# Kernel optimization log

Hardware: AMD Instinct MI355X
Metric: run time of the kernel (lower is better)

The kernel has to match this reference:

```python
import jax, jax.numpy as jnp
import numpy as np

B, T, N = 1024, 256, 64  # batch, seq_len, n_labels


def setup_inputs() -> dict:
    key = jax.random.key(0)
    k1, k2, k3, k4, k5 = jax.random.split(key, 5)
    emit = jax.random.normal(k1, (B, T, N), dtype=jnp.float32)
    lens = jax.random.randint(k2, (B,), T // 2, T + 1)
    mask = jnp.arange(T)[None, :] < lens[:, None]  # [B, T] bool, monotone
    trans = 0.1 * jax.random.normal(k3, (N, N), dtype=jnp.float32)
    strans = 0.1 * jax.random.normal(k4, (N,), dtype=jnp.float32)
    etrans = 0.1 * jax.random.normal(k5, (N,), dtype=jnp.float32)
    return {"emit": emit, "trans": trans, "strans": strans,
            "etrans": etrans, "mask": mask}


def reference(emit, trans, strans, etrans, mask):
    """CRF partition function (Tagger.get_logZ), summed over the batch."""
    lse = jax.scipy.special.logsumexp
    # row-normalize transitions in log space (as in the torch module)
    strans_n = strans - lse(strans)
    etrans_n = etrans - lse(etrans)
    trans_n = trans - lse(trans, axis=-1, keepdims=True)  # [N, N]

    e = jnp.transpose(emit, (1, 0, 2))  # [T, B, N]
    m = mask.T                          # [T, B]

    alpha0 = strans_n + e[0]            # [B, N]

    def step(alpha, xs):
        emit_t, mask_t = xs             # [B, N], [B]
        # scores[b, k] = logsumexp_j(alpha[b, j] + trans[j, k] + emit_t[b, k])
        scores = lse(alpha[:, :, None] + trans_n[None, :, :]
                     + emit_t[:, None, :], axis=1)
        alpha = jnp.where(mask_t[:, None], scores, alpha)
        return alpha, None

    alpha, _ = jax.lax.scan(step, alpha0, (e[1:], m[1:]))
    logZ = jnp.sum(lse(alpha + etrans_n, axis=1))
    return logZ
```

## Files before the change

kernel.cpp:

```cpp
#include <hip/hip_runtime.h>


#define CRF_B 1024
#define CRF_T 256
#define CRF_N 64

typedef __bf16 bf16x2 __attribute__((ext_vector_type(2)));

__device__ __forceinline__ float rl0(float x) {
    return __int_as_float(__builtin_amdgcn_readfirstlane(__float_as_int(x)));
}
__device__ __forceinline__ float rlanef(float x, int j) {
    return __int_as_float(__builtin_amdgcn_readlane(__float_as_int(x), j));
}

__device__ __forceinline__ float wave_lse(float v) {
    float m = v;
    #pragma unroll
    for (int off = 1; off < 64; off <<= 1) m = fmaxf(m, __shfl_xor(m, off));
    float s = __expf(v - m);
    #pragma unroll
    for (int off = 1; off < 64; off <<= 1) s += __shfl_xor(s, off);
    return m + __logf(s);
}

__device__ __forceinline__ unsigned bf16_rne(float f) {
    unsigned u = __float_as_uint(f);
    return (u + 0x7FFFu + ((u >> 16) & 1u)) >> 16;
}

__device__ __forceinline__ float dot2bf(unsigned a, unsigned b, float c) {
#if __has_builtin(__builtin_amdgcn_fdot2_f32_bf16)
    return __builtin_amdgcn_fdot2_f32_bf16(__builtin_bit_cast(bf16x2, a),
                                           __builtin_bit_cast(bf16x2, b),
                                           c, false);
#else
    float d = c;
    asm("v_dot2_f32_bf16 %0, %1, %2, %0" : "+v"(d) : "v"(a), "v"(b));
    return d;
#endif
}

__launch_bounds__(64, 1)
__global__ void crf_fwd_kernel(const float* __restrict__ emit,
                               const float* __restrict__ trans,
                               const float* __restrict__ strans,
                               const float* __restrict__ etrans,
                               const unsigned char* __restrict__ mask_u8,
                               float* __restrict__ out)
{
    const int lane = threadIdx.x;
    const int b    = blockIdx.x;

    __shared__ __attribute__((aligned(16))) unsigned s_up[32];

    float rowlse_v;
    {
        const float* rowp = trans + lane * CRF_N;
        float m = -1e30f;
        #pragma unroll 8
        for (int k = 0; k < CRF_N; ++k) m = fmaxf(m, rowp[k]);
        float s = 0.f;
        #pragma unroll 8
        for (int k = 0; k < CRF_N; ++k) s += __expf(rowp[k] - m);
        rowlse_v = m + __logf(s);
    }

    float cmx = -1e30f;
    #pragma unroll
    for (int j = 0; j < CRF_N; ++j)
        cmx = fmaxf(cmx, trans[j * CRF_N + lane] - rlanef(rowlse_v, j));

    unsigned Epk[32];
    #pragma unroll
    for (int m = 0; m < 32; ++m) {
        float e0 = __expf(trans[(2 * m)     * CRF_N + lane] - rlanef(rowlse_v, 2 * m)     - cmx);
        float e1 = __expf(trans[(2 * m + 1) * CRF_N + lane] - rlanef(rowlse_v, 2 * m + 1) - cmx);
        Epk[m] = bf16_rne(e0) | (bf16_rne(e1) << 16);
    }

    const float sn = wave_lse(strans[lane]);

    int len;
    {
        int c8 = 0;
        #pragma unroll
        for (int q = 0; q < 4; ++q)
            c8 += (mask_u8[(size_t)b * CRF_T + q * 64 + lane] != 0) ? 1 : 0;
        for (int off = 1; off < 64; off <<= 1) c8 += __shfl_xor(c8, off);
        if (c8 >= 128) {
            len = c8;
        } else {
            const int* mi = (const int*)mask_u8;
            int ci = 0;
            #pragma unroll
            for (int q = 0; q < 4; ++q)
                ci += (mi[(size_t)b * CRF_T + q * 64 + lane] != 0) ? 1 : 0;
            for (int off = 1; off < 64; off <<= 1) ci += __shfl_xor(ci, off);
            len = ci;
        }
    }

    const float* eb = emit + (size_t)b * CRF_T * CRF_N;

    float alpha0 = (strans[lane] - sn) + eb[lane];
    float c0 = rl0(alpha0);
    float u  = __expf(alpha0 - c0);
    ((unsigned short*)s_up)[lane] =
        (unsigned short)((__float_as_uint(u) + 0x8000u) >> 16);
    float R  = 1.0f;
    float Pm = 1.0f;
    int   Eacc = 0;

#define CRF_STEP(EE, EE0)                                                   \
    {                                                                       \
        float ree = R * (EE);               \
        float sc0 = R * (EE0);                                              \
        float a0 = 0.f, a1 = 0.f, a2 = 0.f, a3 = 0.f;                       \
        _Pragma("unroll")                                                   \
        for (int m2 = 0; m2 < 32; m2 += 4) {                                \
            uint4 w = *(const uint4*)&s_up[m2];     \
            a0 = dot2bf(w.x, Epk[m2 + 0], a0);                              \
            a1 = dot2bf(w.y, Epk[m2 + 1], a1);                              \
            a2 = dot2bf(w.z, Epk[m2 + 2], a2);                              \
            a3 = dot2bf(w.w, Epk[m2 + 3], a3);                              \
        }                                                                   \
        float s = (a0 + a1) + (a2 + a3);                                    \
        float s0 = rl0(s);                                                  \
        u = s * ree;                                                        \
        ((unsigned short*)s_up)[lane] =                                     \
            (unsigned short)((__float_as_uint(u) + 0x8000u) >> 16);         \
        float u0 = s0 * sc0;              \
        R = __builtin_amdgcn_rcpf(u0);                                      \
        Pm *= u0;                                                           \
    }

    float eN[4], eeC[4], ee0C[4];
    #pragma unroll
    for (int d = 0; d < 4; ++d) eN[d] = eb[(size_t)(1 + d) * CRF_N + lane];
    #pragma unroll
    for (int d = 0; d < 4; ++d) eeC[d] = __expf(eN[d] + cmx);
    #pragma unroll
    for (int d = 0; d < 4; ++d) ee0C[d] = rl0(eeC[d]);

    int t0 = 1;
    while (t0 + 4 <= len) {
        #pragma unroll
        for (int d = 0; d < 4; ++d) {
            int ti = t0 + 4 + d;
            ti = (ti < len) ? ti : (len - 1);
            eN[d] = eb[(size_t)ti * CRF_N + lane];
        }
        CRF_STEP(eeC[0], ee0C[0]); CRF_STEP(eeC[1], ee0C[1]);
        CRF_STEP(eeC[2], ee0C[2]); CRF_STEP(eeC[3], ee0C[3]);
        {
            int ex;
            Pm = frexpf(Pm, &ex);
            Eacc += ex;
        }
        #pragma unroll
        for (int d = 0; d < 4; ++d) eeC[d] = __expf(eN[d] + cmx);
        #pragma unroll
        for (int d = 0; d < 4; ++d) ee0C[d] = rl0(eeC[d]);
        t0 += 4;
    }
    {
        const int nrem = len - t0;
        #pragma unroll
        for (int d = 0; d < 4; ++d) {
            if (d >= nrem) break;
            CRF_STEP(eeC[d], ee0C[d]);
        }
    }
#undef CRF_STEP

    const float en = wave_lse(etrans[lane]);
    float Lacc = c0 + 0.6931471805599453f * (float)Eacc + __logf(Pm);
    float v = Lacc + __logf(u * R) + (etrans[lane] - en);
    float m = v;
    #pragma unroll
    for (int off = 1; off < 64; off <<= 1) m = fmaxf(m, __shfl_xor(m, off));
    float sum = __expf(v - m);
    #pragma unroll
    for (int off = 1; off < 64; off <<= 1) sum += __shfl_xor(sum, off);

    if (lane == 0) {
        atomicAdd(out, m + __logf(sum));
    }
}

extern "C" void kernel_launch(void* const* d_in, const int* in_sizes, int n_in,
                              void* d_out, int out_size, void* d_ws, size_t ws_size,
                              hipStream_t stream) {
    const float* emit   = (const float*)d_in[0];
    const float* trans  = (const float*)d_in[1];
    const float* strans = (const float*)d_in[2];
    const float* etrans = (const float*)d_in[3];
    const unsigned char* mask = (const unsigned char*)d_in[4];
    float* out = (float*)d_out;

    hipMemsetAsync(out, 0, sizeof(float), stream);
    crf_fwd_kernel<<<dim3(CRF_B), dim3(64), 0, stream>>>(
        emit, trans, strans, etrans, mask, out);
}
```

Measured before the change: 144.5 us.

## Split CRF matvec between readlane broadcast and LDS, deepen emission prefetch

Each step now builds packed bf16 pairs in registers with a DPP swap and a perm. The first half of the 64-element dot product takes its operands through scalar readlane broadcasts, while the second half still reads LDS; the LDS write moves to the start of the step. This aims to hide LDS store-to-load latency on the serial recurrence, and the dot products now run over eight accumulators instead of four. Emission loads are also prefetched one group further ahead and interleaved step by step with the exp and readfirstlane work. In exchange it adds many readlane instructions per step and relies on the LDS write being visible to the wave's own later LDS reads without an explicit barrier.

```diff
diff --git a/kernel.cpp b/kernel.cpp
--- a/kernel.cpp
+++ b/kernel.cpp
@@ -27,6 +27,13 @@
 __device__ __forceinline__ unsigned bf16_rne(float f) {
     unsigned u = __float_as_uint(f);
     return (u + 0x7FFFu + ((u >> 16) & 1u)) >> 16;
+}
+
+__device__ __forceinline__ unsigned pack_pairs(float u) {
+    unsigned pa = __float_as_uint(u) + 0x8000u;
+    unsigned pb = (unsigned)__builtin_amdgcn_update_dpp(
+        0, (int)pa, 0xB1 , 0xF, 0xF, false);
+    return __builtin_amdgcn_perm(pb, pa, 0x07060302);
 }
 
 __device__ __forceinline__ float dot2bf(unsigned a, unsigned b, float c) {
@@ -116,25 +123,68 @@
     {                                                                       \
         float ree = R * (EE);               \
         float sc0 = R * (EE0);                                              \
+           \
+        ((unsigned short*)s_up)[lane] =                                     \
+            (unsigned short)((__float_as_uint(u) + 0x8000u) >> 16);         \
+        unsigned upi_ = pack_pairs(u);                                      \
+                           \
+        uint4 w4 = *(const uint4*)&s_up[16];                                \
+        uint4 w5 = *(const uint4*)&s_up[20];                                \
+        uint4 w6 = *(const uint4*)&s_up[24];                                \
+        uint4 w7 = *(const uint4*)&s_up[28];                                \
         float a0 = 0.f, a1 = 0.f, a2 = 0.f, a3 = 0.f;                       \
-        _Pragma("unroll")                                                   \
-        for (int m2 = 0; m2 < 32; m2 += 4) {                                \
-            uint4 w = *(const uint4*)&s_up[m2];     \
-            a0 = dot2bf(w.x, Epk[m2 + 0], a0);                              \
-            a1 = dot2bf(w.y, Epk[m2 + 1], a1);                              \
-            a2 = dot2bf(w.z, Epk[m2 + 2], a2);                              \
-            a3 = dot2bf(w.w, Epk[m2 + 3], a3);                              \
-        }                                                                   \
-        float s = (a0 + a1) + (a2 + a3);                                    \
+        float a4 = 0.f, a5 = 0.f, a6 = 0.f, a7 = 0.f;                       \
+                                    \
+        a0 = dot2bf((unsigned)__builtin_amdgcn_readlane((int)upi_,  0), Epk[ 0], a0); \
+        a1 = dot2bf((unsigned)__builtin_amdgcn_readlane((int)upi_,  2), Epk[ 1], a1); \
+        a2 = dot2bf((unsigned)__builtin_amdgcn_readlane((int)upi_,  4), Epk[ 2], a2); \
+        a3 = dot2bf((unsigned)__builtin_amdgcn_readlane((int)upi_,  6), Epk[ 3], a3); \
+        a4 = dot2bf((unsigned)__builtin_amdgcn_readlane((int)upi_,  8), Epk[ 4], a4); \
+        a5 = dot2bf((unsigned)__builtin_amdgcn_readlane((int)upi_, 10), Epk[ 5], a5); \
+        a6 = dot2bf((unsigned)__builtin_amdgcn_readlane((int)upi_, 12), Epk[ 6], a6); \
+        a7 = dot2bf((unsigned)__builtin_amdgcn_readlane((int)upi_, 14), Epk[ 7], a7); \
+        a0 = dot2bf((unsigned)__builtin_amdgcn_readlane((int)upi_, 16), Epk[ 8], a0); \
+        a1 = dot2bf((unsigned)__builtin_amdgcn_readlane((int)upi_, 18), Epk[ 9], a1); \
+        a2 = dot2bf((unsigned)__builtin_amdgcn_readlane((int)upi_, 20), Epk[10], a2); \
+        a3 = dot2bf((unsigned)__builtin_amdgcn_readlane((int)upi_, 22), Epk[11], a3); \
+        a4 = dot2bf((unsigned)__builtin_amdgcn_readlane((int)upi_, 24), Epk[12], a4); \
+        a5 = dot2bf((unsigned)__builtin_amdgcn_readlane((int)upi_, 26), Epk[13], a5); \
+        a6 = dot2bf((unsigned)__builtin_amdgcn_readlane((int)upi_, 28), Epk[14], a6); \
+        a7 = dot2bf((unsigned)__builtin_amdgcn_readlane((int)upi_, 30), Epk[15], a7); \
+            \
+        a0 = dot2bf(w4.x, Epk[16], a0);                                     \
+        a1 = dot2bf(w4.y, Epk[17], a1);                                     \
+        a2 = dot2bf(w4.z, Epk[18], a2);                                     \
+        a3 = dot2bf(w4.w, Epk[19], a3);                                     \
+        a4 = dot2bf(w5.x, Epk[20], a4);                                     \
+        a5 = dot2bf(w5.y, Epk[21], a5);                                     \
+        a6 = dot2bf(w5.z, Epk[22], a6);                                     \
+        a7 = dot2bf(w5.w, Epk[23], a7);                                     \
+        a0 = dot2bf(w6.x, Epk[24], a0);                                     \
+        a1 = dot2bf(w6.y, Epk[25], a1);                                     \
+        a2 = dot2bf(w6.z, Epk[26], a2);                                     \
+        a3 = dot2bf(w6.w, Epk[27], a3);                                     \
+        a4 = dot2bf(w7.x, Epk[28], a4);                                     \
+        a5 = dot2bf(w7.y, Epk[29], a5);                                     \
+        a6 = dot2bf(w7.z, Epk[30], a6);                                     \
+        a7 = dot2bf(w7.w, Epk[31], a7);                                     \
+        float s = (((a0 + a1) + (a2 + a3)) + ((a4 + a5) + (a6 + a7)));      \
         float s0 = rl0(s);                                                  \
         u = s * ree;                                                        \
-        ((unsigned short*)s_up)[lane] =                                     \
-            (unsigned short)((__float_as_uint(u) + 0x8000u) >> 16);         \
         float u0 = s0 * sc0;              \
         R = __builtin_amdgcn_rcpf(u0);                                      \
         Pm *= u0;                                                           \
     }
 
+#define CRF_ROT(D)                                                          \
+    {                                                                       \
+        eeC[D]  = __expf(eN[D] + cmx);                                      \
+        ee0C[D] = rl0(eeC[D]);                                              \
+        int ti = t0 + 8 + (D);                                              \
+        ti = (ti < len) ? ti : (len - 1);                                   \
+        eN[D] = eb[(size_t)ti * CRF_N + lane];                              \
+    }
+
     float eN[4], eeC[4], ee0C[4];
     #pragma unroll
     for (int d = 0; d < 4; ++d) eN[d] = eb[(size_t)(1 + d) * CRF_N + lane];
@@ -142,26 +192,20 @@
     for (int d = 0; d < 4; ++d) eeC[d] = __expf(eN[d] + cmx);
     #pragma unroll
     for (int d = 0; d < 4; ++d) ee0C[d] = rl0(eeC[d]);
+    #pragma unroll
+    for (int d = 0; d < 4; ++d) eN[d] = eb[(size_t)(5 + d) * CRF_N + lane];
 
     int t0 = 1;
     while (t0 + 4 <= len) {
-        #pragma unroll
-        for (int d = 0; d < 4; ++d) {
-            int ti = t0 + 4 + d;
-            ti = (ti < len) ? ti : (len - 1);
-            eN[d] = eb[(size_t)ti * CRF_N + lane];
-        }
-        CRF_STEP(eeC[0], ee0C[0]); CRF_STEP(eeC[1], ee0C[1]);
-        CRF_STEP(eeC[2], ee0C[2]); CRF_STEP(eeC[3], ee0C[3]);
+        CRF_STEP(eeC[0], ee0C[0]); CRF_ROT(0);
+        CRF_STEP(eeC[1], ee0C[1]); CRF_ROT(1);
+        CRF_STEP(eeC[2], ee0C[2]); CRF_ROT(2);
+        CRF_STEP(eeC[3], ee0C[3]); CRF_ROT(3);
         {
             int ex;
             Pm = frexpf(Pm, &ex);
             Eacc += ex;
         }
-        #pragma unroll
-        for (int d = 0; d < 4; ++d) eeC[d] = __expf(eN[d] + cmx);
-        #pragma unroll
-        for (int d = 0; d < 4; ++d) ee0C[d] = rl0(eeC[d]);
         t0 += 4;
     }
     {
@@ -173,6 +217,7 @@
         }
     }
 #undef CRF_STEP
+#undef CRF_ROT
 
     const float en = wave_lse(etrans[lane]);
     float Lacc = c0 + 0.6931471805599453f * (float)Eacc + __logf(Pm);
```

Measured after the change: 150.5 us. 4.2% more time.

## Split alpha broadcast between DPP/readlane and LDS paths within each step

Applied to the files above, without the earlier changes.

Each recurrence step now writes the bf16 alpha to LDS and immediately issues the reads for the upper 32 labels in inline asm. Meanwhile the lower 32 labels are packed into bf16 pairs with a DPP swap plus perm and broadcast via readlane, so half the dot products overlap the LDS round-trip latency. The write now happens at the start of the next step instead of the end of the current one. This relies on inline asm ordering within a single wave with no barrier, and adds many scalar readlane operations to the serial critical path.

```diff
diff --git a/kernel.cpp b/kernel.cpp
--- a/kernel.cpp
+++ b/kernel.cpp
@@ -27,6 +27,12 @@
 __device__ __forceinline__ unsigned bf16_rne(float f) {
     unsigned u = __float_as_uint(f);
     return (u + 0x7FFFu + ((u >> 16) & 1u)) >> 16;
+}
+
+__device__ __forceinline__ unsigned pack_pairs_pa(unsigned pa) {
+    unsigned pb = (unsigned)__builtin_amdgcn_update_dpp(
+        0, (int)pa, 0xB1 , 0xF, 0xF, false);
+    return __builtin_amdgcn_perm(pb, pa, 0x07060302);
 }
 
 __device__ __forceinline__ float dot2bf(unsigned a, unsigned b, float c) {
@@ -53,6 +59,10 @@
     const int b    = blockIdx.x;
 
     __shared__ __attribute__((aligned(16))) unsigned s_up[32];
+
+    const unsigned lds_base = (unsigned)(unsigned long long)(&s_up[0]);
+    const unsigned lds_wr   = lds_base + (unsigned)lane * 2u;
+    const unsigned lds_rd   = lds_base + 64u;
 
     float rowlse_v;
     {
@@ -106,8 +116,6 @@
     float alpha0 = (strans[lane] - sn) + eb[lane];
     float c0 = rl0(alpha0);
     float u  = __expf(alpha0 - c0);
-    ((unsigned short*)s_up)[lane] =
-        (unsigned short)((__float_as_uint(u) + 0x8000u) >> 16);
     float R  = 1.0f;
     float Pm = 1.0f;
     int   Eacc = 0;
@@ -116,20 +124,55 @@
     {                                                                       \
         float ree = R * (EE);               \
         float sc0 = R * (EE0);                                              \
+        unsigned pa_ = __float_as_uint(u) + 0x8000u;                        \
+        uint4 w4, w5, w6, w7;                                               \
+        asm volatile(                                                       \
+            "ds_write_b16 %5, %6\n\t"                                       \
+            "ds_read_b128 %0, %4 offset:0\n\t"                              \
+            "ds_read_b128 %1, %4 offset:16\n\t"                             \
+            "ds_read_b128 %2, %4 offset:32\n\t"                             \
+            "ds_read_b128 %3, %4 offset:48"                                 \
+            : "=&v"(w4), "=&v"(w5), "=&v"(w6), "=&v"(w7)                    \
+            : "v"(lds_rd), "v"(lds_wr), "v"(pa_ >> 16)                      \
+            : "memory");                                                    \
+        unsigned upi_ = pack_pairs_pa(pa_);                                 \
         float a0 = 0.f, a1 = 0.f, a2 = 0.f, a3 = 0.f;                       \
+        float a4 = 0.f, a5 = 0.f, a6 = 0.f, a7 = 0.f;                       \
+                      \
         _Pragma("unroll")                                                   \
-        for (int m2 = 0; m2 < 32; m2 += 4) {                                \
-            uint4 w = *(const uint4*)&s_up[m2];     \
-            a0 = dot2bf(w.x, Epk[m2 + 0], a0);                              \
-            a1 = dot2bf(w.y, Epk[m2 + 1], a1);                              \
-            a2 = dot2bf(w.z, Epk[m2 + 2], a2);                              \
-            a3 = dot2bf(w.w, Epk[m2 + 3], a3);                              \
+        for (int m2 = 0; m2 < 16; m2 += 4) {                                \
+            unsigned q0 = (unsigned)__builtin_amdgcn_readlane((int)upi_, 2 * m2 + 0); \
+            unsigned q1 = (unsigned)__builtin_amdgcn_readlane((int)upi_, 2 * m2 + 2); \
+            unsigned q2 = (unsigned)__builtin_amdgcn_readlane((int)upi_, 2 * m2 + 4); \
+            unsigned q3 = (unsigned)__builtin_amdgcn_readlane((int)upi_, 2 * m2 + 6); \
+            a0 = dot2bf(q0, Epk[m2 + 0], a0);                               \
+            a1 = dot2bf(q1, Epk[m2 + 1], a1);                               \
+            a2 = dot2bf(q2, Epk[m2 + 2], a2);                               \
+            a3 = dot2bf(q3, Epk[m2 + 3], a3);                               \
         }                                                                   \
-        float s = (a0 + a1) + (a2 + a3);                                    \
+          \
+        asm volatile("s_waitcnt lgkmcnt(0)" ::: "memory");                  \
+        __builtin_amdgcn_sched_barrier(0);                                  \
+                         \
+        a4 = dot2bf(w4.x, Epk[16], a4);                                     \
+        a5 = dot2bf(w4.y, Epk[17], a5);                                     \
+        a6 = dot2bf(w4.z, Epk[18], a6);                                     \
+        a7 = dot2bf(w4.w, Epk[19], a7);                                     \
+        a4 = dot2bf(w5.x, Epk[20], a4);                                     \
+        a5 = dot2bf(w5.y, Epk[21], a5);                                     \
+        a6 = dot2bf(w5.z, Epk[22], a6);                                     \
+        a7 = dot2bf(w5.w, Epk[23], a7);                                     \
+        a4 = dot2bf(w6.x, Epk[24], a4);                                     \
+        a5 = dot2bf(w6.y, Epk[25], a5);                                     \
+        a6 = dot2bf(w6.z, Epk[26], a6);                                     \
+        a7 = dot2bf(w6.w, Epk[27], a7);                                     \
+        a4 = dot2bf(w7.x, Epk[28], a4);                                     \
+        a5 = dot2bf(w7.y, Epk[29], a5);                                     \
+        a6 = dot2bf(w7.z, Epk[30], a6);                                     \
+        a7 = dot2bf(w7.w, Epk[31], a7);                                     \
+        float s = (((a0 + a1) + (a2 + a3)) + ((a4 + a5) + (a6 + a7)));      \
         float s0 = rl0(s);                                                  \
         u = s * ree;                                                        \
-        ((unsigned short*)s_up)[lane] =                                     \
-            (unsigned short)((__float_as_uint(u) + 0x8000u) >> 16);         \
         float u0 = s0 * sc0;              \
         R = __builtin_amdgcn_rcpf(u0);                                      \
         Pm *= u0;                                                           \
```

Measured after the change: 147.5 us. +2.1%, slower.

## Split recurrence dot product between register readlanes and early-issued LDS reads

Applied to the files above, without the earlier changes.

Each recurrence step now gets the first 24 alpha values straight from registers, using a DPP swap, a byte permute and scalar readlanes. The remaining values are read from LDS with ds_read_b128 instructions issued at the start of the step. The register-sourced dot products run while the LDS reads are in flight, so less LDS latency sits on the serial per-timestep critical path. The LDS write and the wait are hand-placed in inline asm with a sched_barrier, which adds scalar readlane work and hard-coded LDS offsets that are fragile.

```diff
diff --git a/kernel.cpp b/kernel.cpp
--- a/kernel.cpp
+++ b/kernel.cpp
@@ -27,6 +27,12 @@
 __device__ __forceinline__ unsigned bf16_rne(float f) {
     unsigned u = __float_as_uint(f);
     return (u + 0x7FFFu + ((u >> 16) & 1u)) >> 16;
+}
+
+__device__ __forceinline__ unsigned pack_pairs_pa(unsigned pa) {
+    unsigned pb = (unsigned)__builtin_amdgcn_update_dpp(
+        0, (int)pa, 0xB1 , 0xF, 0xF, false);
+    return __builtin_amdgcn_perm(pb, pa, 0x07060302);
 }
 
 __device__ __forceinline__ float dot2bf(unsigned a, unsigned b, float c) {
@@ -53,6 +59,10 @@
     const int b    = blockIdx.x;
 
     __shared__ __attribute__((aligned(16))) unsigned s_up[32];
+
+    const unsigned lds_base = (unsigned)(unsigned long long)(&s_up[0]);
+    const unsigned lds_wr   = lds_base + (unsigned)lane * 2u;
+    const unsigned lds_rd   = lds_base + 48u;
 
     float rowlse_v;
     {
@@ -106,30 +116,89 @@
     float alpha0 = (strans[lane] - sn) + eb[lane];
     float c0 = rl0(alpha0);
     float u  = __expf(alpha0 - c0);
-    ((unsigned short*)s_up)[lane] =
-        (unsigned short)((__float_as_uint(u) + 0x8000u) >> 16);
+    {
+        unsigned pa0 = __float_as_uint(u) + 0x8000u;
+        asm volatile("ds_write_b16 %0, %1" :: "v"(lds_wr), "v"(pa0 >> 16) : "memory");
+    }
     float R  = 1.0f;
     float Pm = 1.0f;
     int   Eacc = 0;
 
 #define CRF_STEP(EE, EE0)                                                   \
     {                                                                       \
+        uint4 wA, wB, wC, wD, wE;                                           \
+        asm volatile(                                                       \
+            "ds_read_b128 %0, %5 offset:0\n\t"                              \
+            "ds_read_b128 %1, %5 offset:16\n\t"                             \
+            "ds_read_b128 %2, %5 offset:32\n\t"                             \
+            "ds_read_b128 %3, %5 offset:48\n\t"                             \
+            "ds_read_b128 %4, %5 offset:64"                                 \
+            : "=&v"(wA), "=&v"(wB), "=&v"(wC), "=&v"(wD), "=&v"(wE)         \
+            : "v"(lds_rd)                                                   \
+            : "memory");                                                    \
         float ree = R * (EE);               \
         float sc0 = R * (EE0);                                              \
+        unsigned pa_ = __float_as_uint(u) + 0x8000u;                        \
+        unsigned upi_ = pack_pairs_pa(pa_);                                 \
         float a0 = 0.f, a1 = 0.f, a2 = 0.f, a3 = 0.f;                       \
-        _Pragma("unroll")                                                   \
-        for (int m2 = 0; m2 < 32; m2 += 4) {                                \
-            uint4 w = *(const uint4*)&s_up[m2];     \
-            a0 = dot2bf(w.x, Epk[m2 + 0], a0);                              \
-            a1 = dot2bf(w.y, Epk[m2 + 1], a1);                              \
-            a2 = dot2bf(w.z, Epk[m2 + 2], a2);                              \
-            a3 = dot2bf(w.w, Epk[m2 + 3], a3);                              \
-        }                                                                   \
-        float s = (a0 + a1) + (a2 + a3);                                    \
+        float a4 = 0.f, a5 = 0.f, a6 = 0.f, a7 = 0.f;                       \
+                    \
+        unsigned q0  = (unsigned)__builtin_amdgcn_readlane((int)upi_,  0);  \
+        unsigned q1  = (unsigned)__builtin_amdgcn_readlane((int)upi_,  2);  \
+        unsigned q2  = (unsigned)__builtin_amdgcn_readlane((int)upi_,  4);  \
+        unsigned q3  = (unsigned)__builtin_amdgcn_readlane((int)upi_,  6);  \
+        unsigned q4  = (unsigned)__builtin_amdgcn_readlane((int)upi_,  8);  \
+        unsigned q5  = (unsigned)__builtin_amdgcn_readlane((int)upi_, 10);  \
+        unsigned q6  = (unsigned)__builtin_amdgcn_readlane((int)upi_, 12);  \
+        unsigned q7  = (unsigned)__builtin_amdgcn_readlane((int)upi_, 14);  \
+        unsigned q8  = (unsigned)__builtin_amdgcn_readlane((int)upi_, 16);  \
+        unsigned q9  = (unsigned)__builtin_amdgcn_readlane((int)upi_, 18);  \
+        unsigned q10 = (unsigned)__builtin_amdgcn_readlane((int)upi_, 20);  \
+        unsigned q11 = (unsigned)__builtin_amdgcn_readlane((int)upi_, 22);  \
+        a0 = dot2bf(q0,  Epk[ 0], a0);                                      \
+        a1 = dot2bf(q1,  Epk[ 1], a1);                                      \
+        a2 = dot2bf(q2,  Epk[ 2], a2);                                      \
+        a3 = dot2bf(q3,  Epk[ 3], a3);                                      \
+        a0 = dot2bf(q4,  Epk[ 4], a0);                                      \
+        a1 = dot2bf(q5,  Epk[ 5], a1);                                      \
+        a2 = dot2bf(q6,  Epk[ 6], a2);                                      \
+        a3 = dot2bf(q7,  Epk[ 7], a3);                                      \
+        a0 = dot2bf(q8,  Epk[ 8], a0);                                      \
+        a1 = dot2bf(q9,  Epk[ 9], a1);                                      \
+        a2 = dot2bf(q10, Epk[10], a2);                                      \
+        a3 = dot2bf(q11, Epk[11], a3);                                      \
+          \
+        asm volatile("s_waitcnt lgkmcnt(0)" ::: "memory");                  \
+        __builtin_amdgcn_sched_barrier(0);                                  \
+                                 \
+        a4 = dot2bf(wA.x, Epk[12], a4);                                     \
+        a5 = dot2bf(wA.y, Epk[13], a5);                                     \
+        a6 = dot2bf(wA.z, Epk[14], a6);                                     \
+        a7 = dot2bf(wA.w, Epk[15], a7);                                     \
+        a4 = dot2bf(wB.x, Epk[16], a4);                                     \
+        a5 = dot2bf(wB.y, Epk[17], a5);                                     \
+        a6 = dot2bf(wB.z, Epk[18], a6);                                     \
+        a7 = dot2bf(wB.w, Epk[19], a7);                                     \
+        a4 = dot2bf(wC.x, Epk[20], a4);                                     \
+        a5 = dot2bf(wC.y, Epk[21], a5);                                     \
+        a6 = dot2bf(wC.z, Epk[22], a6);                                     \
+        a7 = dot2bf(wC.w, Epk[23], a7);                                     \
+        a4 = dot2bf(wD.x, Epk[24], a4);                                     \
+        a5 = dot2bf(wD.y, Epk[25], a5);                                     \
+        a6 = dot2bf(wD.z, Epk[26], a6);                                     \
+        a7 = dot2bf(wD.w, Epk[27], a7);                                     \
+        a4 = dot2bf(wE.x, Epk[28], a4);                                     \
+        a5 = dot2bf(wE.y, Epk[29], a5);                                     \
+        a6 = dot2bf(wE.z, Epk[30], a6);                                     \
+        a7 = dot2bf(wE.w, Epk[31], a7);                                     \
+        float s = (((a0 + a1) + (a2 + a3)) + ((a4 + a5) + (a6 + a7)));      \
+        u = s * ree;                                                        \
+          \
+        unsigned pw_ = __float_as_uint(u) + 0x8000u;                        \
+        asm volatile("ds_write_b16 %0, %1" :: "v"(lds_wr), "v"(pw_ >> 16)   \
+                     : "memory");                                           \
+                           \
         float s0 = rl0(s);                                                  \
-        u = s * ree;                                                        \
-        ((unsigned short*)s_up)[lane] =                                     \
-            (unsigned short)((__float_as_uint(u) + 0x8000u) >> 16);         \
         float u0 = s0 * sc0;              \
         R = __builtin_amdgcn_rcpf(u0);                                      \
         Pm *= u0;                                                           \
```

After: 148.9 us. 1.03x slower.
